# Kernel tuning notes

Hardware: AMD Instinct MI355X
Metric: run time of the kernel (lower is better)

The kernel has to match this reference:

```python
import jax, jax.numpy as jnp
import numpy as np

KSIZE = 5
PAD = 2  # replicate padding per side for 'same' 5x5x5 box filter


def setup_inputs() -> dict:
    key = jax.random.key(0)
    # mp: [N, C, D, H, W] nonnegative probability maps
    mp = jax.random.uniform(key, (1, 21, 16, 256, 256), dtype=jnp.float32)
    return {"mp": mp}


def reference(mp):
    N, C, D, H, W = mp.shape
    # replicate ('edge') padding on D, H, W, then depthwise 5x5x5 box filter
    x = jnp.pad(mp, ((0, 0), (0, 0), (PAD, PAD), (PAD, PAD), (PAD, PAD)), mode="edge")
    k = jnp.full((C, 1, KSIZE, KSIZE, KSIZE), 1.0 / (KSIZE ** 3), dtype=mp.dtype)
    y = jax.lax.conv_general_dilated(
        x, k,
        window_strides=(1, 1, 1),
        padding="VALID",
        dimension_numbers=("NCDHW", "OIDHW", "NCDHW"),
        feature_group_count=C,
    )  # [N, C, D, H, W]

    # normalize over channel axis (torch permutes to put channels first; we keep axis=1)
    y = y / jnp.sum(y, axis=1, keepdims=True)

    # weighted-median selection: running cumulative sum over channels
    s = jnp.cumsum(y, axis=1)                     # [N, C, D, H, W]
    idx = jnp.arange(C).reshape(1, C, 1, 1, 1)    # channel indices

    # med0: LAST channel i with y[i] > 0 and cumsum < 0.5 (torch loop overwrites), default 0
    med0 = jnp.maximum(
        jnp.max(jnp.where((y > 0) & (s < 0.5), idx, -1), axis=1, keepdims=True), 0
    )
    # med1: torch sets med[1] only while med[1]==0, so the result is the FIRST
    # NONZERO channel with cumsum > 0.5 (i=0 qualifying leaves med[1]==0 and gets
    # overwritten by the next qualifying i); 0 if no nonzero channel qualifies.
    med1 = jnp.argmax((s > 0.5) & (idx > 0), axis=1, keepdims=True)

    keep = (idx == med0) | (idx == med1)
    return jnp.where(keep, y, jnp.zeros((), dtype=y.dtype))
```

## Files before the change

kernel.cpp:

```cpp
#include <hip/hip_runtime.h>

#define CC   21
#define DD   16
#define HH   256
#define WW   256
#define HWP  (HH * WW)
#define DHW  (DD * HWP)

#define TW   32
#define TH   8
#define PYN  12
#define AROW 36
#define A_SZ (DD * PYN * AROW)

typedef float f4u __attribute__((ext_vector_type(4), aligned(8)));

__device__ __forceinline__ f4u f4add(f4u a, f4u b) { return a + b; }

__global__ __launch_bounds__(256, 5) void blur_kernel(const float* __restrict__ mp,
                                                      float* __restrict__ out) {
    __shared__ float A[A_SZ];

    const int w0 = blockIdx.x * TW;
    const int h0 = blockIdx.y * TH;
    const int ch = blockIdx.z;
    const int tid = threadIdx.x;
    const float* __restrict__ src = mp + (size_t)ch * DHW;

    if (tid < 216) {
        const int s   = (tid >= 108) ? 1 : 0;
        const int col = tid - s * 108;
        const int py  = col / 9;
        const int jjq = col - py * 9;
        const int h   = min(HH - 1, max(0, h0 + py - 2));
        int lw = w0 - 2 + jjq * 4;
        const bool lo = (lw < 0);
        const bool hi = (lw > WW - 4);
        lw = lo ? 0 : (hi ? (WW - 4) : lw);
        const float* colp = src + h * WW + lw;

        f4u l[12];
#pragma unroll
        for (int m = 0; m < 12; ++m) {
            int dz = s * 8 + m;
            int d  = min(DD - 1, max(0, dz - 2));
            l[m] = *(const f4u*)(colp + (size_t)d * HWP);
        }
        f4u sum = f4add(f4add(f4add(l[0], l[1]), f4add(l[2], l[3])), l[4]);
#pragma unroll
        for (int i = 0; i < 8; ++i) {
            f4u o = sum;
            if (lo) o = f4u{o.x, o.x, o.x, o.y};
            if (hi) o = f4u{o.z, o.w, o.w, o.w};
            *(f4u*)(&A[((s * 8 + i) * PYN + py) * AROW + jjq * 4]) = o;
            if (i < 7) sum = sum - l[i] + l[i + 5];
        }
    }
    __syncthreads();

#pragma unroll
    for (int it = 0; it < 2; ++it) {
        const int t    = tid + it * 256;
        const int y    = t & 7;
        const int quad = (t >> 3) & 3;
        const int dout = t >> 5;
        const int x0   = quad * 8;

        const float* base = &A[(dout * PYN + y) * AROW + x0];
        f4u A0 = *(const f4u*)(base);
        f4u A1 = *(const f4u*)(base + 4);
        f4u A2 = *(const f4u*)(base + 8);
#pragma unroll
        for (int k = 1; k < 5; ++k) {
            base += AROW;
            A0 = f4add(A0, *(const f4u*)(base));
            A1 = f4add(A1, *(const f4u*)(base + 4));
            A2 = f4add(A2, *(const f4u*)(base + 8));
        }
        float hs[12] = {A0.x, A0.y, A0.z, A0.w, A1.x, A1.y, A1.z, A1.w,
                        A2.x, A2.y, A2.z, A2.w};
        float4 o0, o1;
        o0.x = hs[0] + hs[1] + hs[2] + hs[3] + hs[4];
        o0.y = hs[1] + hs[2] + hs[3] + hs[4] + hs[5];
        o0.z = hs[2] + hs[3] + hs[4] + hs[5] + hs[6];
        o0.w = hs[3] + hs[4] + hs[5] + hs[6] + hs[7];
        o1.x = hs[4] + hs[5] + hs[6] + hs[7] + hs[8];
        o1.y = hs[5] + hs[6] + hs[7] + hs[8] + hs[9];
        o1.z = hs[6] + hs[7] + hs[8] + hs[9] + hs[10];
        o1.w = hs[7] + hs[8] + hs[9] + hs[10] + hs[11];

        float* dst = out + (size_t)ch * DHW + (size_t)dout * HWP
                   + (h0 + y) * WW + w0 + x0;
        *(float4*)(dst)     = o0;
        *(float4*)(dst + 4) = o1;
    }
}

__global__ __launch_bounds__(256) void median_kernel(float* __restrict__ y4) {
    const size_t i = (size_t)blockIdx.x * 256 + threadIdx.x;
    const size_t base = i * 4;

    float v[CC][4];
    float tot[4] = {0.f, 0.f, 0.f, 0.f};
#pragma unroll
    for (int c = 0; c < CC; ++c) {
        float4 t = *(const float4*)(y4 + (size_t)c * DHW + base);
        v[c][0] = t.x; v[c][1] = t.y; v[c][2] = t.z; v[c][3] = t.w;
#pragma unroll
        for (int p = 0; p < 4; ++p) tot[p] += v[c][p];
    }
    float inv[4];
#pragma unroll
    for (int p = 0; p < 4; ++p) inv[p] = 1.0f / tot[p];

    float s[4] = {0.f, 0.f, 0.f, 0.f};
    float v0[4], v1[4];
    int m0[4] = {0, 0, 0, 0}, m1[4] = {0, 0, 0, 0};
#pragma unroll
    for (int c = 0; c < CC; ++c) {
#pragma unroll
        for (int p = 0; p < 4; ++p) {
            float yn = v[c][p] * inv[p];
            float sn = s[p] + yn;
            if (c == 0) { v0[p] = yn; v1[p] = yn; }
            if (v[c][p] > 0.f && sn < 0.5f) { m0[p] = c; v0[p] = yn; }
            if (m1[p] == 0 && c > 0 && sn > 0.5f) { m1[p] = c; v1[p] = yn; }
            s[p] = sn;
        }
    }

#pragma unroll
    for (int c = 0; c < CC; ++c) {
        float4 o;
        o.x = (c == m0[0]) ? v0[0] : ((c == m1[0]) ? v1[0] : 0.f);
        o.y = (c == m0[1]) ? v0[1] : ((c == m1[1]) ? v1[1] : 0.f);
        o.z = (c == m0[2]) ? v0[2] : ((c == m1[2]) ? v1[2] : 0.f);
        o.w = (c == m0[3]) ? v0[3] : ((c == m1[3]) ? v1[3] : 0.f);
        *(float4*)(y4 + (size_t)c * DHW + base) = o;
    }
}

extern "C" void kernel_launch(void* const* d_in, const int* in_sizes, int n_in,
                              void* d_out, int out_size, void* d_ws, size_t ws_size,
                              hipStream_t stream) {
    const float* mp = (const float*)d_in[0];
    float* out = (float*)d_out;

    dim3 bgrid(WW / TW, HH / TH, CC);
    blur_kernel<<<bgrid, 256, 0, stream>>>(mp, out);

    median_kernel<<<(DHW / 4) / 256, 256, 0, stream>>>(out);
}
```

Measured before the change: 198.8 us.

## Move W-axis box sum from blur kernel into median kernel

The blur kernel now computes only the D and H sums, writing aligned 16-byte tiles without horizontal halo handling or edge shuffles. The W-direction 5-tap sum is moved into the median kernel, which stages one H row of all 21 channels in shared memory with replicated edge padding, then runs the weighted-median selection one pixel per thread. This removes the unaligned halo loads and the 12-element horizontal sum from the blur stage. In exchange the median kernel gains shared-memory staging, a barrier and scalar rather than float4 stores.

```diff
diff --git a/kernel.cpp b/kernel.cpp
--- a/kernel.cpp
+++ b/kernel.cpp
@@ -7,136 +7,115 @@
 #define HWP  (HH * WW)
 #define DHW  (DD * HWP)
 
-#define TW   32
-#define TH   8
+typedef float f4a __attribute__((ext_vector_type(4), aligned(16)));
+__device__ __forceinline__ f4a f4add(f4a a, f4a b) { return a + b; }
+
+#define AROW 36
 #define PYN  12
-#define AROW 36
 #define A_SZ (DD * PYN * AROW)
 
-typedef float f4u __attribute__((ext_vector_type(4), aligned(8)));
-
-__device__ __forceinline__ f4u f4add(f4u a, f4u b) { return a + b; }
-
-__global__ __launch_bounds__(256, 5) void blur_kernel(const float* __restrict__ mp,
-                                                      float* __restrict__ out) {
+__global__ __launch_bounds__(256, 5) void dh_blur_kernel(const float* __restrict__ mp,
+                                                         float* __restrict__ out) {
     __shared__ float A[A_SZ];
 
-    const int w0 = blockIdx.x * TW;
-    const int h0 = blockIdx.y * TH;
+    const int w0 = blockIdx.x * 32;
+    const int h0 = blockIdx.y * 8;
     const int ch = blockIdx.z;
     const int tid = threadIdx.x;
     const float* __restrict__ src = mp + (size_t)ch * DHW;
 
-    if (tid < 216) {
-        const int s   = (tid >= 108) ? 1 : 0;
-        const int col = tid - s * 108;
-        const int py  = col / 9;
-        const int jjq = col - py * 9;
+    if (tid < 192) {
+        const int s   = (tid >= 96) ? 1 : 0;
+        const int col = tid - s * 96;
+        const int py  = col >> 3;
+        const int x4  = col & 7;
         const int h   = min(HH - 1, max(0, h0 + py - 2));
-        int lw = w0 - 2 + jjq * 4;
-        const bool lo = (lw < 0);
-        const bool hi = (lw > WW - 4);
-        lw = lo ? 0 : (hi ? (WW - 4) : lw);
-        const float* colp = src + h * WW + lw;
+        const float* colp = src + (size_t)h * WW + w0 + x4 * 4;
 
-        f4u l[12];
+        f4a l[12];
 #pragma unroll
         for (int m = 0; m < 12; ++m) {
             int dz = s * 8 + m;
             int d  = min(DD - 1, max(0, dz - 2));
-            l[m] = *(const f4u*)(colp + (size_t)d * HWP);
+            l[m] = *(const f4a*)(colp + (size_t)d * HWP);
         }
-        f4u sum = f4add(f4add(f4add(l[0], l[1]), f4add(l[2], l[3])), l[4]);
+        f4a sum = f4add(f4add(f4add(l[0], l[1]), f4add(l[2], l[3])), l[4]);
 #pragma unroll
         for (int i = 0; i < 8; ++i) {
-            f4u o = sum;
-            if (lo) o = f4u{o.x, o.x, o.x, o.y};
-            if (hi) o = f4u{o.z, o.w, o.w, o.w};
-            *(f4u*)(&A[((s * 8 + i) * PYN + py) * AROW + jjq * 4]) = o;
+            *(f4a*)(&A[((s * 8 + i) * PYN + py) * AROW + x4 * 4]) = sum;
             if (i < 7) sum = sum - l[i] + l[i + 5];
         }
     }
     __syncthreads();
 
 #pragma unroll
-    for (int it = 0; it < 2; ++it) {
+    for (int it = 0; it < 4; ++it) {
         const int t    = tid + it * 256;
-        const int y    = t & 7;
-        const int quad = (t >> 3) & 3;
-        const int dout = t >> 5;
-        const int x0   = quad * 8;
+        const int x4   = t & 7;
+        const int y    = (t >> 3) & 7;
+        const int dout = t >> 6;
 
-        const float* base = &A[(dout * PYN + y) * AROW + x0];
-        f4u A0 = *(const f4u*)(base);
-        f4u A1 = *(const f4u*)(base + 4);
-        f4u A2 = *(const f4u*)(base + 8);
+        const float* b = &A[(dout * PYN + y) * AROW + x4 * 4];
+        f4a a = *(const f4a*)b;
 #pragma unroll
-        for (int k = 1; k < 5; ++k) {
-            base += AROW;
-            A0 = f4add(A0, *(const f4u*)(base));
-            A1 = f4add(A1, *(const f4u*)(base + 4));
-            A2 = f4add(A2, *(const f4u*)(base + 8));
-        }
-        float hs[12] = {A0.x, A0.y, A0.z, A0.w, A1.x, A1.y, A1.z, A1.w,
-                        A2.x, A2.y, A2.z, A2.w};
-        float4 o0, o1;
-        o0.x = hs[0] + hs[1] + hs[2] + hs[3] + hs[4];
-        o0.y = hs[1] + hs[2] + hs[3] + hs[4] + hs[5];
-        o0.z = hs[2] + hs[3] + hs[4] + hs[5] + hs[6];
-        o0.w = hs[3] + hs[4] + hs[5] + hs[6] + hs[7];
-        o1.x = hs[4] + hs[5] + hs[6] + hs[7] + hs[8];
-        o1.y = hs[5] + hs[6] + hs[7] + hs[8] + hs[9];
-        o1.z = hs[6] + hs[7] + hs[8] + hs[9] + hs[10];
-        o1.w = hs[7] + hs[8] + hs[9] + hs[10] + hs[11];
+        for (int k = 1; k < 5; ++k) a = f4add(a, *(const f4a*)(b + k * AROW));
 
-        float* dst = out + (size_t)ch * DHW + (size_t)dout * HWP
-                   + (h0 + y) * WW + w0 + x0;
-        *(float4*)(dst)     = o0;
-        *(float4*)(dst + 4) = o1;
+        *(f4a*)(out + (size_t)ch * DHW + (size_t)dout * HWP
+                + (h0 + y) * WW + w0 + x4 * 4) = a;
     }
 }
 
-__global__ __launch_bounds__(256) void median_kernel(float* __restrict__ y4) {
-    const size_t i = (size_t)blockIdx.x * 256 + threadIdx.x;
-    const size_t base = i * 4;
+#define ROWP 264
 
-    float v[CC][4];
-    float tot[4] = {0.f, 0.f, 0.f, 0.f};
+__global__ __launch_bounds__(256) void wmedian_kernel(float* __restrict__ y4) {
+    __shared__ float R[CC * ROWP];
+
+    const int h = blockIdx.x;
+    const int d = blockIdx.y;
+    const int tid = threadIdx.x;
+    float* __restrict__ base = y4 + (size_t)d * HWP + (size_t)h * WW;
+
+    for (int idx = tid; idx < CC * 64; idx += 256) {
+        const int c  = idx >> 6;
+        const int w4 = idx & 63;
+        *(f4a*)(&R[c * ROWP + 4 + w4 * 4]) = *(const f4a*)(base + (size_t)c * DHW + w4 * 4);
+    }
+    if (tid < CC) {
+        const float v0 = base[(size_t)tid * DHW];
+        const float vL = base[(size_t)tid * DHW + (WW - 1)];
+        R[tid * ROWP + 2]   = v0;
+        R[tid * ROWP + 3]   = v0;
+        R[tid * ROWP + 260] = vL;
+        R[tid * ROWP + 261] = vL;
+    }
+    __syncthreads();
+
+    const int w = tid;
+    float v[CC];
+    float tot = 0.f;
 #pragma unroll
     for (int c = 0; c < CC; ++c) {
-        float4 t = *(const float4*)(y4 + (size_t)c * DHW + base);
-        v[c][0] = t.x; v[c][1] = t.y; v[c][2] = t.z; v[c][3] = t.w;
-#pragma unroll
-        for (int p = 0; p < 4; ++p) tot[p] += v[c][p];
+        const float* r = &R[c * ROWP + 2 + w];
+        v[c] = ((((r[0] + r[1]) + r[2]) + r[3]) + r[4]);
+        tot += v[c];
     }
-    float inv[4];
-#pragma unroll
-    for (int p = 0; p < 4; ++p) inv[p] = 1.0f / tot[p];
+    const float inv = 1.0f / tot;
 
-    float s[4] = {0.f, 0.f, 0.f, 0.f};
-    float v0[4], v1[4];
-    int m0[4] = {0, 0, 0, 0}, m1[4] = {0, 0, 0, 0};
+    float s = 0.f, sv0 = 0.f, sv1 = 0.f;
+    int m0 = 0, m1 = 0;
 #pragma unroll
     for (int c = 0; c < CC; ++c) {
-#pragma unroll
-        for (int p = 0; p < 4; ++p) {
-            float yn = v[c][p] * inv[p];
-            float sn = s[p] + yn;
-            if (c == 0) { v0[p] = yn; v1[p] = yn; }
-            if (v[c][p] > 0.f && sn < 0.5f) { m0[p] = c; v0[p] = yn; }
-            if (m1[p] == 0 && c > 0 && sn > 0.5f) { m1[p] = c; v1[p] = yn; }
-            s[p] = sn;
-        }
+        const float yn = v[c] * inv;
+        const float sn = s + yn;
+        if (c == 0) { sv0 = yn; sv1 = yn; }
+        if (v[c] > 0.f && sn < 0.5f) { m0 = c; sv0 = yn; }
+        if (m1 == 0 && c > 0 && sn > 0.5f) { m1 = c; sv1 = yn; }
+        s = sn;
     }
 
 #pragma unroll
     for (int c = 0; c < CC; ++c) {
-        float4 o;
-        o.x = (c == m0[0]) ? v0[0] : ((c == m1[0]) ? v1[0] : 0.f);
-        o.y = (c == m0[1]) ? v0[1] : ((c == m1[1]) ? v1[1] : 0.f);
-        o.z = (c == m0[2]) ? v0[2] : ((c == m1[2]) ? v1[2] : 0.f);
-        o.w = (c == m0[3]) ? v0[3] : ((c == m1[3]) ? v1[3] : 0.f);
-        *(float4*)(y4 + (size_t)c * DHW + base) = o;
+        base[(size_t)c * DHW + w] = (c == m0) ? sv0 : ((c == m1) ? sv1 : 0.f);
     }
 }
 
@@ -146,8 +125,6 @@
     const float* mp = (const float*)d_in[0];
     float* out = (float*)d_out;
 
-    dim3 bgrid(WW / TW, HH / TH, CC);
-    blur_kernel<<<bgrid, 256, 0, stream>>>(mp, out);
-
-    median_kernel<<<(DHW / 4) / 256, 256, 0, stream>>>(out);
+    dh_blur_kernel<<<dim3(WW / 32, HH / 8, CC), 256, 0, stream>>>(mp, out);
+    wmedian_kernel<<<dim3(HH, DD), 256, 0, stream>>>(out);
 }
```

Result: no change. 194.9 us (-1.9%).
